# Kernel optimization log

Measured on AMD Instinct MI355X. Metric: run time of the kernel, lower is better.

Reference implementation:

```python
import jax, jax.numpy as jnp
import numpy as np

N_NODES = 50000
N_EDGES = 600000
IN_DIM, HID_DIM, OUT_DIM = 128, 256, 40


def setup_inputs() -> dict:
    key = jax.random.key(0)
    ks = jax.random.split(key, 10)
    x = jax.random.normal(ks[0], (N_NODES, IN_DIM), dtype=jnp.float32)
    edge_index = jax.random.randint(ks[1], (2, N_EDGES), 0, N_NODES, dtype=jnp.int64)
    def lin(k, out_d, in_d):
        s = 1.0 / np.sqrt(in_d)
        return jax.random.uniform(k, (out_d, in_d), jnp.float32, -s, s)
    # SAGEConv: lin_l (on aggregated neighbors, with bias) + lin_r (on self, no bias)
    params = {
        "Wl1": lin(ks[2], HID_DIM, IN_DIM), "bl1": jnp.zeros((HID_DIM,), jnp.float32), "Wr1": lin(ks[3], HID_DIM, IN_DIM),
        "Wl2": lin(ks[4], HID_DIM, HID_DIM), "bl2": jnp.zeros((HID_DIM,), jnp.float32), "Wr2": lin(ks[5], HID_DIM, HID_DIM),
        "Wl3": lin(ks[6], OUT_DIM, HID_DIM), "bl3": jnp.zeros((OUT_DIM,), jnp.float32), "Wr3": lin(ks[7], OUT_DIM, HID_DIM),
    }
    return {"x": x, "edge_index": edge_index, **params}


def _sage_conv(x, src, dst, Wl, bl, Wr):
    # mean-aggregate source features into destination nodes
    n = x.shape[0]
    agg = jax.ops.segment_sum(x[src], dst, num_segments=n)          # [N, d_in]
    cnt = jax.ops.segment_sum(jnp.ones_like(dst, dtype=x.dtype), dst, num_segments=n)
    mean = agg / jnp.maximum(cnt, 1.0)[:, None]
    return mean @ Wl.T + bl + x @ Wr.T


def reference(x, edge_index, Wl1, bl1, Wr1, Wl2, bl2, Wr2, Wl3, bl3, Wr3):
    src, dst = edge_index[0], edge_index[1]
    h = _sage_conv(x, src, dst, Wl1, bl1, Wr1)
    h = jax.nn.relu(h)  # dropout is identity in eval mode
    h = _sage_conv(h, src, dst, Wl2, bl2, Wr2)
    h = jax.nn.relu(h)
    h = _sage_conv(h, src, dst, Wl3, bl3, Wr3)
    return jax.nn.log_softmax(h, axis=1)
```

## Files before the change

### kernel.cpp

```cpp
#include <hip/hip_runtime.h>
#include <hip/hip_bf16.h>

#define IN_DIM 128
#define HID_DIM 256
#define OUT_DIM 40
#define SCAN_CHUNK 2048

typedef __attribute__((ext_vector_type(8))) __bf16 bf16x8;
typedef __attribute__((ext_vector_type(4))) float f32x4;

__device__ inline ushort f2bf(float f) {
    uint u = __builtin_bit_cast(uint, f);
    u = (u + 0x7fff + ((u >> 16) & 1)) >> 16;
    return (ushort)u;
}
__device__ inline float bfl(uint u) { return __builtin_bit_cast(float, u << 16); }
__device__ inline float bfh(uint u) { return __builtin_bit_cast(float, u & 0xffff0000u); }

__global__ __launch_bounds__(256) void cvt_x(const float* __restrict__ in,
                                             ushort* __restrict__ out, int n4) {
    int i = blockIdx.x * 256 + threadIdx.x;
    if (i < n4) {
        float4 v = ((const float4*)in)[i];
        uint2 o;
        o.x = (uint)f2bf(v.x) | ((uint)f2bf(v.y) << 16);
        o.y = (uint)f2bf(v.z) | ((uint)f2bf(v.w) << 16);
        ((uint2*)out)[i] = o;
    }
}

__global__ __launch_bounds__(256) void cvt_w2(const float* __restrict__ wl,
                                              const float* __restrict__ wr,
                                              ushort* __restrict__ ol,
                                              ushort* __restrict__ orr,
                                              int O, int OPAD, int K) {
    int idx = blockIdx.x * 256 + threadIdx.x;
    int tot = OPAD * K;
    if (idx >= tot) return;
    int row = idx / K;
    int col = idx - row * K;
    ushort vl = 0, vr = 0;
    if (row < O) {
        vl = f2bf(wl[row * K + col]);
        vr = f2bf(wr[row * K + col]);
    }
    ol[idx] = vl;
    orr[idx] = vr;
}

__global__ __launch_bounds__(256) void hist_kernel(const int* __restrict__ dst,
                                                   int* __restrict__ cnt, int E) {
    int e = blockIdx.x * 256 + threadIdx.x;
    if (e < E) atomicAdd(&cnt[dst[e]], 1);
}

__global__ __launch_bounds__(256) void scan_pass1(const int* __restrict__ cnt,
                                                  int* __restrict__ bsum, int N) {
    __shared__ int red[256];
    const int base = blockIdx.x * SCAN_CHUNK;
    int s = 0;
    for (int i = threadIdx.x; i < SCAN_CHUNK; i += 256) {
        int idx = base + i;
        if (idx < N) s += cnt[idx];
    }
    red[threadIdx.x] = s;
    __syncthreads();
    for (int o = 128; o > 0; o >>= 1) {
        if (threadIdx.x < o) red[threadIdx.x] += red[threadIdx.x + o];
        __syncthreads();
    }
    if (threadIdx.x == 0) bsum[blockIdx.x] = red[0];
}

__global__ __launch_bounds__(256) void scan_pass2(int* __restrict__ bsum, int B) {
    __shared__ int ls[256];
    const int t = threadIdx.x;
    int v = (t < B) ? bsum[t] : 0;
    ls[t] = v;
    __syncthreads();
    for (int o = 1; o < 256; o <<= 1) {
        int u = (t >= o) ? ls[t - o] : 0;
        __syncthreads();
        ls[t] += u;
        __syncthreads();
    }
    if (t < B) bsum[t] = ls[t] - v;
}

__global__ __launch_bounds__(256) void scan_pass3(const int* __restrict__ cnt,
                                                  const int* __restrict__ bsum,
                                                  int* __restrict__ rowptr,
                                                  int* __restrict__ cursor,
                                                  float* __restrict__ inv, int N, int E) {
    __shared__ int ls[256];
    const int tbase = blockIdx.x * SCAN_CHUNK + threadIdx.x * 8;
    int c[8];
    int s = 0;
#pragma unroll
    for (int j = 0; j < 8; ++j) {
        int idx = tbase + j;
        c[j] = (idx < N) ? cnt[idx] : 0;
        s += c[j];
    }
    ls[threadIdx.x] = s;
    __syncthreads();
    for (int o = 1; o < 256; o <<= 1) {
        int u = (threadIdx.x >= o) ? ls[threadIdx.x - o] : 0;
        __syncthreads();
        ls[threadIdx.x] += u;
        __syncthreads();
    }
    int run = bsum[blockIdx.x] + ls[threadIdx.x] - s;
#pragma unroll
    for (int j = 0; j < 8; ++j) {
        int idx = tbase + j;
        if (idx < N) {
            rowptr[idx] = run;
            cursor[idx] = run;
            inv[idx] = 1.0f / fmaxf((float)c[j], 1.0f);
            run += c[j];
        }
    }
    if (blockIdx.x == 0 && threadIdx.x == 0) rowptr[N] = E;
}

__global__ __launch_bounds__(256) void fill_kernel(const int* __restrict__ src,
                                                   const int* __restrict__ dst,
                                                   int* __restrict__ cursor,
                                                   int* __restrict__ srcs, int E) {
    int e = blockIdx.x * 256 + threadIdx.x;
    if (e < E) {
        int pos = atomicAdd(&cursor[dst[e]], 1);
        srcs[pos] = src[e];
    }
}

template <int D>
__global__ __launch_bounds__(256) void gather_mean_bf(const ushort* __restrict__ feat,
                                                      const int* __restrict__ rowptr,
                                                      const int* __restrict__ srcs,
                                                      const float* __restrict__ inv,
                                                      ushort* __restrict__ out, int N) {
    constexpr int V = D / 64;
    const int wave = threadIdx.x >> 6;
    const int lane = threadIdx.x & 63;
    const int n = blockIdx.x * 4 + wave;
    if (n >= N) return;
    const int beg = rowptr[n];
    const int end = rowptr[n + 1];
    const int col = lane * V;
    float a0 = 0.f, a1 = 0.f, a2 = 0.f, a3 = 0.f;
    int e = beg;
    if constexpr (V == 4) {
        for (; e + 3 < end; e += 4) {
            int s0 = srcs[e], s1 = srcs[e + 1], s2 = srcs[e + 2], s3 = srcs[e + 3];
            uint2 q0 = *(const uint2*)&feat[(long long)s0 * D + col];
            uint2 q1 = *(const uint2*)&feat[(long long)s1 * D + col];
            uint2 q2 = *(const uint2*)&feat[(long long)s2 * D + col];
            uint2 q3 = *(const uint2*)&feat[(long long)s3 * D + col];
            a0 += (bfl(q0.x) + bfl(q1.x)) + (bfl(q2.x) + bfl(q3.x));
            a1 += (bfh(q0.x) + bfh(q1.x)) + (bfh(q2.x) + bfh(q3.x));
            a2 += (bfl(q0.y) + bfl(q1.y)) + (bfl(q2.y) + bfl(q3.y));
            a3 += (bfh(q0.y) + bfh(q1.y)) + (bfh(q2.y) + bfh(q3.y));
        }
        for (; e + 1 < end; e += 2) {
            int s0 = srcs[e], s1 = srcs[e + 1];
            uint2 q0 = *(const uint2*)&feat[(long long)s0 * D + col];
            uint2 q1 = *(const uint2*)&feat[(long long)s1 * D + col];
            a0 += bfl(q0.x) + bfl(q1.x);
            a1 += bfh(q0.x) + bfh(q1.x);
            a2 += bfl(q0.y) + bfl(q1.y);
            a3 += bfh(q0.y) + bfh(q1.y);
        }
        if (e < end) {
            uint2 q0 = *(const uint2*)&feat[(long long)srcs[e] * D + col];
            a0 += bfl(q0.x); a1 += bfh(q0.x); a2 += bfl(q0.y); a3 += bfh(q0.y);
        }
        const float sc = inv[n];
        uint2 o;
        o.x = (uint)f2bf(a0 * sc) | ((uint)f2bf(a1 * sc) << 16);
        o.y = (uint)f2bf(a2 * sc) | ((uint)f2bf(a3 * sc) << 16);
        *(uint2*)&out[(long long)n * D + col] = o;
    } else {
        for (; e + 3 < end; e += 4) {
            int s0 = srcs[e], s1 = srcs[e + 1], s2 = srcs[e + 2], s3 = srcs[e + 3];
            uint q0 = *(const uint*)&feat[(long long)s0 * D + col];
            uint q1 = *(const uint*)&feat[(long long)s1 * D + col];
            uint q2 = *(const uint*)&feat[(long long)s2 * D + col];
            uint q3 = *(const uint*)&feat[(long long)s3 * D + col];
            a0 += (bfl(q0) + bfl(q1)) + (bfl(q2) + bfl(q3));
            a1 += (bfh(q0) + bfh(q1)) + (bfh(q2) + bfh(q3));
        }
        for (; e + 1 < end; e += 2) {
            int s0 = srcs[e], s1 = srcs[e + 1];
            uint q0 = *(const uint*)&feat[(long long)s0 * D + col];
            uint q1 = *(const uint*)&feat[(long long)s1 * D + col];
            a0 += bfl(q0) + bfl(q1);
            a1 += bfh(q0) + bfh(q1);
        }
        if (e < end) {
            uint q0 = *(const uint*)&feat[(long long)srcs[e] * D + col];
            a0 += bfl(q0); a1 += bfh(q0);
        }
        const float sc = inv[n];
        uint o = (uint)f2bf(a0 * sc) | ((uint)f2bf(a1 * sc) << 16);
        *(uint*)&out[(long long)n * D + col] = o;
    }
}

template <int K, bool RELU, bool OUTBF>
__global__ __launch_bounds__(256, 2) void sage_gemm_fused(const ushort* __restrict__ Amean,
                                                          const ushort* __restrict__ Aself,
                                                          const ushort* __restrict__ Wl,
                                                          const float* __restrict__ bias,
                                                          const ushort* __restrict__ Wr,
                                                          void* __restrict__ outv, int N, int O) {
    constexpr int K2 = 2 * K;
    constexpr int KP = K2 + 8;
    constexpr int NK = K2 / 32;
    __shared__ __align__(16) ushort Ws[64 * KP];

    const int tid = threadIdx.x;
    const int wave = tid >> 6;
    const int lane = tid & 63;
    const int ln = lane & 15;
    const int quad = lane >> 4;
    const int bm0 = (blockIdx.x >> 2) * 128;
    const int bn0 = (blockIdx.x & 3) * 64;

    int arow[2];
#pragma unroll
    for (int rt = 0; rt < 2; ++rt) {
        int r = bm0 + wave * 32 + rt * 16 + ln;
        arow[rt] = min(r, N - 1);
    }

#pragma unroll
    for (int i = tid; i < 64 * (K / 8); i += 256) {
        int row = i / (K / 8);
        int c8 = (i % (K / 8)) * 8;
        *(ulonglong2*)&Ws[row * KP + c8] =
            *(const ulonglong2*)&Wl[(long long)(bn0 + row) * K + c8];
        *(ulonglong2*)&Ws[row * KP + K + c8] =
            *(const ulonglong2*)&Wr[(long long)(bn0 + row) * K + c8];
    }

    f32x4 acc[2][4] = {};
    bf16x8 a_cur[2], a_nxt[2];
#pragma unroll
    for (int rt = 0; rt < 2; ++rt)
        a_cur[rt] = *(const bf16x8*)&Amean[(long long)arow[rt] * K + quad * 8];

    __syncthreads();

#pragma unroll
    for (int kk = 0; kk < NK; ++kk) {
        if (kk + 1 < NK) {
            const ushort* __restrict__ An = (kk + 1 < NK / 2) ? Amean : Aself;
            const int ko = ((kk + 1) % (NK / 2)) * 32;
#pragma unroll
            for (int rt = 0; rt < 2; ++rt)
                a_nxt[rt] = *(const bf16x8*)&An[(long long)arow[rt] * K + ko + quad * 8];
        }
#pragma unroll
        for (int ct = 0; ct < 4; ++ct) {
            bf16x8 b = *(const bf16x8*)&Ws[(ct * 16 + ln) * KP + kk * 32 + quad * 8];
#pragma unroll
            for (int rt = 0; rt < 2; ++rt)
                acc[rt][ct] = __builtin_amdgcn_mfma_f32_16x16x32_bf16(a_cur[rt], b, acc[rt][ct], 0, 0, 0);
        }
#pragma unroll
        for (int rt = 0; rt < 2; ++rt) a_cur[rt] = a_nxt[rt];
    }

#pragma unroll
    for (int rt = 0; rt < 2; ++rt) {
        int rbase = bm0 + wave * 32 + rt * 16 + quad * 4;
#pragma unroll
        for (int ct = 0; ct < 4; ++ct) {
            int col = bn0 + ct * 16 + ln;
            if (col >= O) continue;
            float bv = bias[col];
#pragma unroll
            for (int r = 0; r < 4; ++r) {
                int row = rbase + r;
                if (row >= N) continue;
                float v = acc[rt][ct][r] + bv;
                if (RELU) v = fmaxf(v, 0.f);
                if (OUTBF)
                    ((ushort*)outv)[(long long)row * O + col] = f2bf(v);
                else
                    ((float*)outv)[(long long)row * O + col] = v;
            }
        }
    }
}

template <int K>
__global__ __launch_bounds__(256, 2) void sage_gemm_pre(const ushort* __restrict__ A0,
                                                        const ushort* __restrict__ Wl,
                                                        const ushort* __restrict__ Wr,
                                                        ushort* __restrict__ P,
                                                        float* __restrict__ S, int N, int O) {
    constexpr int KP = 2 * K + 8;
    constexpr int NK = K / 32;
    __shared__ __align__(16) ushort Ws[64 * KP];

    const int tid = threadIdx.x;
    const int wave = tid >> 6;
    const int lane = tid & 63;
    const int ln = lane & 15;
    const int quad = lane >> 4;
    const int bm0 = blockIdx.x * 64;

    const int arow = min(bm0 + wave * 16 + ln, N - 1);

    bf16x8 areg[NK];
#pragma unroll
    for (int kk = 0; kk < NK; ++kk)
        areg[kk] = *(const bf16x8*)&A0[(long long)arow * K + kk * 32 + quad * 8];

#pragma unroll
    for (int i = tid; i < 64 * (K / 8); i += 256) {
        int row = i / (K / 8);
        int c8 = (i % (K / 8)) * 8;
        *(ulonglong2*)&Ws[row * KP + c8] =
            *(const ulonglong2*)&Wl[(long long)row * K + c8];
        *(ulonglong2*)&Ws[row * KP + K + c8] =
            *(const ulonglong2*)&Wr[(long long)row * K + c8];
    }
    __syncthreads();

#pragma unroll
    for (int phase = 0; phase < 2; ++phase) {
        f32x4 acc[4] = {};
#pragma unroll
        for (int kk = 0; kk < NK; ++kk) {
#pragma unroll
            for (int ct = 0; ct < 4; ++ct) {
                bf16x8 b = *(const bf16x8*)&Ws[(ct * 16 + ln) * KP + phase * K + kk * 32 + quad * 8];
                acc[ct] = __builtin_amdgcn_mfma_f32_16x16x32_bf16(areg[kk], b, acc[ct], 0, 0, 0);
            }
        }
        int rbase = bm0 + wave * 16 + quad * 4;
#pragma unroll
        for (int ct = 0; ct < 3; ++ct) {
            int col = ct * 16 + ln;
            if (col >= O) continue;
#pragma unroll
            for (int r = 0; r < 4; ++r) {
                int row = rbase + r;
                if (row >= N) continue;
                if (phase == 0)
                    P[(long long)row * O + col] = f2bf(acc[ct][r]);
                else
                    S[(long long)row * O + col] = acc[ct][r];
            }
        }
    }
}

__global__ __launch_bounds__(256) void agg_bias_lsm(const ushort* __restrict__ P,
                                                    const float* __restrict__ S,
                                                    const float* __restrict__ bias,
                                                    const int* __restrict__ rowptr,
                                                    const int* __restrict__ srcs,
                                                    const float* __restrict__ inv,
                                                    float* __restrict__ out, int N) {
    const int wave = threadIdx.x >> 6;
    const int lane = threadIdx.x & 63;
    const int n = blockIdx.x * 4 + wave;
    if (n >= N) return;
    const int beg = rowptr[n];
    const int end = rowptr[n + 1];
    const bool act = lane < OUT_DIM;
    const int cidx = act ? lane : 0;

    float acc = 0.f;
    int e = beg;
    for (; e + 3 < end; e += 4) {
        int s0 = srcs[e], s1 = srcs[e + 1], s2 = srcs[e + 2], s3 = srcs[e + 3];
        float v0 = __builtin_bit_cast(float, (uint)P[(long long)s0 * OUT_DIM + cidx] << 16);
        float v1 = __builtin_bit_cast(float, (uint)P[(long long)s1 * OUT_DIM + cidx] << 16);
        float v2 = __builtin_bit_cast(float, (uint)P[(long long)s2 * OUT_DIM + cidx] << 16);
        float v3 = __builtin_bit_cast(float, (uint)P[(long long)s3 * OUT_DIM + cidx] << 16);
        acc += (v0 + v1) + (v2 + v3);
    }
    for (; e < end; ++e)
        acc += __builtin_bit_cast(float, (uint)P[(long long)srcs[e] * OUT_DIM + cidx] << 16);

    float v = act ? (acc * inv[n] + S[(long long)n * OUT_DIM + lane] + bias[lane]) : -INFINITY;
    float m = v;
#pragma unroll
    for (int o = 32; o > 0; o >>= 1) m = fmaxf(m, __shfl_xor(m, o, 64));
    float ex = act ? expf(v - m) : 0.f;
    float sm = ex;
#pragma unroll
    for (int o = 32; o > 0; o >>= 1) sm += __shfl_xor(sm, o, 64);
    float ls = logf(sm);
    if (act) out[(long long)n * OUT_DIM + lane] = v - m - ls;
}

extern "C" void kernel_launch(void* const* d_in, const int* in_sizes, int n_in,
                              void* d_out, int out_size, void* d_ws, size_t ws_size,
                              hipStream_t stream) {
    const float* x   = (const float*)d_in[0];
    const int*   ei  = (const int*)d_in[1];
    const float* Wl1 = (const float*)d_in[2];
    const float* bl1 = (const float*)d_in[3];
    const float* Wr1 = (const float*)d_in[4];
    const float* Wl2 = (const float*)d_in[5];
    const float* bl2 = (const float*)d_in[6];
    const float* Wr2 = (const float*)d_in[7];
    const float* Wl3 = (const float*)d_in[8];
    const float* bl3 = (const float*)d_in[9];
    const float* Wr3 = (const float*)d_in[10];
    float* out = (float*)d_out;

    const int N = in_sizes[0] / IN_DIM;
    const int E = in_sizes[1] / 2;
    const int* src = ei;
    const int* dst = ei + E;

    char* w = (char*)d_ws;
    size_t off = 0;
    auto alloc = [&](size_t bytes) {
        void* p = w + off;
        off = (off + bytes + 255) & ~(size_t)255;
        return p;
    };
    ushort* xb   = (ushort*)alloc((size_t)N * IN_DIM * 2);
    ushort* M    = (ushort*)alloc((size_t)N * HID_DIM * 2);
    ushort* H1   = (ushort*)alloc((size_t)N * HID_DIM * 2);
    ushort* H2   = (ushort*)alloc((size_t)N * HID_DIM * 2);
    ushort* P3   = (ushort*)alloc((size_t)N * OUT_DIM * 2);
    float*  S3   = (float*)alloc((size_t)N * OUT_DIM * 4);
    float*  inv  = (float*)alloc((size_t)N * 4);
    int*    cnt  = (int*)alloc((size_t)N * 4);
    int*    rowptr = (int*)alloc((size_t)(N + 1) * 4);
    int*    cursor = (int*)alloc((size_t)N * 4);
    int*    srcs = (int*)alloc((size_t)E * 4);
    int*    bsum = (int*)alloc(256 * 4);
    ushort* Wl1b = (ushort*)alloc(256 * 128 * 2);
    ushort* Wr1b = (ushort*)alloc(256 * 128 * 2);
    ushort* Wl2b = (ushort*)alloc(256 * 256 * 2);
    ushort* Wr2b = (ushort*)alloc(256 * 256 * 2);
    ushort* Wl3b = (ushort*)alloc(64 * 256 * 2);
    ushort* Wr3b = (ushort*)alloc(64 * 256 * 2);

    cvt_x<<<(N * IN_DIM / 4 + 255) / 256, 256, 0, stream>>>(x, xb, N * IN_DIM / 4);
    cvt_w2<<<(256 * 128 + 255) / 256, 256, 0, stream>>>(Wl1, Wr1, Wl1b, Wr1b, 256, 256, 128);
    cvt_w2<<<(256 * 256 + 255) / 256, 256, 0, stream>>>(Wl2, Wr2, Wl2b, Wr2b, 256, 256, 256);
    cvt_w2<<<(64 * 256 + 255) / 256, 256, 0, stream>>>(Wl3, Wr3, Wl3b, Wr3b, 40, 64, 256);

    const int SB = (N + SCAN_CHUNK - 1) / SCAN_CHUNK;
    hipMemsetAsync(cnt, 0, (size_t)N * sizeof(int), stream);
    hist_kernel<<<(E + 255) / 256, 256, 0, stream>>>(dst, cnt, E);
    scan_pass1<<<SB, 256, 0, stream>>>(cnt, bsum, N);
    scan_pass2<<<1, 256, 0, stream>>>(bsum, SB);
    scan_pass3<<<SB, 256, 0, stream>>>(cnt, bsum, rowptr, cursor, inv, N, E);
    fill_kernel<<<(E + 255) / 256, 256, 0, stream>>>(src, dst, cursor, srcs, E);

    const int gm = (N + 127) / 128;
    const int gg = (N + 3) / 4;

    gather_mean_bf<IN_DIM><<<gg, 256, 0, stream>>>(xb, rowptr, srcs, inv, M, N);
    sage_gemm_fused<IN_DIM, true, true><<<gm * 4, 256, 0, stream>>>(
        M, xb, Wl1b, bl1, Wr1b, H1, N, HID_DIM);

    gather_mean_bf<HID_DIM><<<gg, 256, 0, stream>>>(H1, rowptr, srcs, inv, M, N);
    sage_gemm_fused<HID_DIM, true, true><<<gm * 4, 256, 0, stream>>>(
        M, H1, Wl2b, bl2, Wr2b, H2, N, HID_DIM);

    sage_gemm_pre<HID_DIM><<<(N + 63) / 64, 256, 0, stream>>>(
        H2, Wl3b, Wr3b, P3, S3, N, OUT_DIM);
    agg_bias_lsm<<<gg, 256, 0, stream>>>(P3, S3, bl3, rowptr, srcs, inv, out, N);
}
```

Measured before the change: 381.0 us.

## Split fused SAGE GEMM into two K phases to halve shared memory

The fused GEMM now stages only one weight matrix (Wl, then Wr) in shared memory per phase instead of both concatenated, which halves LDS use and raises the occupancy target to 3 blocks per CU. It preloads all A fragments for each phase into registers instead of software-pipelining one step ahead. The grid becomes 2D with column tiles on blockIdx.y, which changes the order in which blocks are dispatched. The layer-3 pre-GEMM trims its padded output columns from 64 to 48, cutting LDS and MFMA work. The trade-offs are an extra pair of barriers and weight reload per block, plus higher register pressure from the full A preload.

```diff
diff --git a/kernel.cpp b/kernel.cpp
--- a/kernel.cpp
+++ b/kernel.cpp
@@ -209,15 +209,14 @@
 }
 
 template <int K, bool RELU, bool OUTBF>
-__global__ __launch_bounds__(256, 2) void sage_gemm_fused(const ushort* __restrict__ Amean,
-                                                          const ushort* __restrict__ Aself,
-                                                          const ushort* __restrict__ Wl,
-                                                          const float* __restrict__ bias,
-                                                          const ushort* __restrict__ Wr,
-                                                          void* __restrict__ outv, int N, int O) {
-    constexpr int K2 = 2 * K;
-    constexpr int KP = K2 + 8;
-    constexpr int NK = K2 / 32;
+__global__ __launch_bounds__(256, 3) void sage_gemm_mfma(const ushort* __restrict__ Amean,
+                                                         const ushort* __restrict__ Aself,
+                                                         const ushort* __restrict__ Wl,
+                                                         const float* __restrict__ bias,
+                                                         const ushort* __restrict__ Wr,
+                                                         void* __restrict__ outv, int N, int O) {
+    constexpr int KP = K + 8;
+    constexpr int NK = K / 32;
     __shared__ __align__(16) ushort Ws[64 * KP];
 
     const int tid = threadIdx.x;
@@ -225,8 +224,8 @@
     const int lane = tid & 63;
     const int ln = lane & 15;
     const int quad = lane >> 4;
-    const int bm0 = (blockIdx.x >> 2) * 128;
-    const int bn0 = (blockIdx.x & 3) * 64;
+    const int bm0 = blockIdx.x * 128;
+    const int bn0 = blockIdx.y * 64;
 
     int arow[2];
 #pragma unroll
@@ -235,42 +234,39 @@
         arow[rt] = min(r, N - 1);
     }
 
-#pragma unroll
-    for (int i = tid; i < 64 * (K / 8); i += 256) {
-        int row = i / (K / 8);
-        int c8 = (i % (K / 8)) * 8;
-        *(ulonglong2*)&Ws[row * KP + c8] =
-            *(const ulonglong2*)&Wl[(long long)(bn0 + row) * K + c8];
-        *(ulonglong2*)&Ws[row * KP + K + c8] =
-            *(const ulonglong2*)&Wr[(long long)(bn0 + row) * K + c8];
-    }
-
     f32x4 acc[2][4] = {};
-    bf16x8 a_cur[2], a_nxt[2];
-#pragma unroll
-    for (int rt = 0; rt < 2; ++rt)
-        a_cur[rt] = *(const bf16x8*)&Amean[(long long)arow[rt] * K + quad * 8];
-
-    __syncthreads();
-
-#pragma unroll
-    for (int kk = 0; kk < NK; ++kk) {
-        if (kk + 1 < NK) {
-            const ushort* __restrict__ An = (kk + 1 < NK / 2) ? Amean : Aself;
-            const int ko = ((kk + 1) % (NK / 2)) * 32;
+
+    for (int phase = 0; phase < 2; ++phase) {
+        const ushort* __restrict__ A = phase ? Aself : Amean;
+        const ushort* __restrict__ W = phase ? Wr : Wl;
+
+        __syncthreads();
+#pragma unroll
+        for (int i = tid; i < 64 * (K / 8); i += 256) {
+            int row = i / (K / 8);
+            int c8 = (i % (K / 8)) * 8;
+            *(ulonglong2*)&Ws[row * KP + c8] =
+                *(const ulonglong2*)&W[(long long)(bn0 + row) * K + c8];
+        }
+        __syncthreads();
+
+        bf16x8 areg[NK][2];
+#pragma unroll
+        for (int kk = 0; kk < NK; ++kk)
 #pragma unroll
             for (int rt = 0; rt < 2; ++rt)
-                a_nxt[rt] = *(const bf16x8*)&An[(long long)arow[rt] * K + ko + quad * 8];
-        }
-#pragma unroll
-        for (int ct = 0; ct < 4; ++ct) {
-            bf16x8 b = *(const bf16x8*)&Ws[(ct * 16 + ln) * KP + kk * 32 + quad * 8];
-#pragma unroll
-            for (int rt = 0; rt < 2; ++rt)
-                acc[rt][ct] = __builtin_amdgcn_mfma_f32_16x16x32_bf16(a_cur[rt], b, acc[rt][ct], 0, 0, 0);
-        }
-#pragma unroll
-        for (int rt = 0; rt < 2; ++rt) a_cur[rt] = a_nxt[rt];
+                areg[kk][rt] = *(const bf16x8*)&A[(long long)arow[rt] * K + kk * 32 + quad * 8];
+
+#pragma unroll
+        for (int kk = 0; kk < NK; ++kk) {
+#pragma unroll
+            for (int ct = 0; ct < 4; ++ct) {
+                bf16x8 b = *(const bf16x8*)&Ws[(ct * 16 + ln) * KP + kk * 32 + quad * 8];
+#pragma unroll
+                for (int rt = 0; rt < 2; ++rt)
+                    acc[rt][ct] = __builtin_amdgcn_mfma_f32_16x16x32_bf16(areg[kk][rt], b, acc[rt][ct], 0, 0, 0);
+            }
+        }
     }
 
 #pragma unroll
@@ -297,14 +293,14 @@
 }
 
 template <int K>
-__global__ __launch_bounds__(256, 2) void sage_gemm_pre(const ushort* __restrict__ A0,
+__global__ __launch_bounds__(256, 3) void sage_gemm_pre(const ushort* __restrict__ A0,
                                                         const ushort* __restrict__ Wl,
                                                         const ushort* __restrict__ Wr,
                                                         ushort* __restrict__ P,
                                                         float* __restrict__ S, int N, int O) {
     constexpr int KP = 2 * K + 8;
     constexpr int NK = K / 32;
-    __shared__ __align__(16) ushort Ws[64 * KP];
+    __shared__ __align__(16) ushort Ws[48 * KP];
 
     const int tid = threadIdx.x;
     const int wave = tid >> 6;
@@ -315,13 +311,8 @@
 
     const int arow = min(bm0 + wave * 16 + ln, N - 1);
 
-    bf16x8 areg[NK];
-#pragma unroll
-    for (int kk = 0; kk < NK; ++kk)
-        areg[kk] = *(const bf16x8*)&A0[(long long)arow * K + kk * 32 + quad * 8];
-
-#pragma unroll
-    for (int i = tid; i < 64 * (K / 8); i += 256) {
+#pragma unroll
+    for (int i = tid; i < 48 * (K / 8); i += 256) {
         int row = i / (K / 8);
         int c8 = (i % (K / 8)) * 8;
         *(ulonglong2*)&Ws[row * KP + c8] =
@@ -331,13 +322,18 @@
     }
     __syncthreads();
 
+    bf16x8 areg[NK];
+#pragma unroll
+    for (int kk = 0; kk < NK; ++kk)
+        areg[kk] = *(const bf16x8*)&A0[(long long)arow * K + kk * 32 + quad * 8];
+
 #pragma unroll
     for (int phase = 0; phase < 2; ++phase) {
-        f32x4 acc[4] = {};
+        f32x4 acc[3] = {};
 #pragma unroll
         for (int kk = 0; kk < NK; ++kk) {
 #pragma unroll
-            for (int ct = 0; ct < 4; ++ct) {
+            for (int ct = 0; ct < 3; ++ct) {
                 bf16x8 b = *(const bf16x8*)&Ws[(ct * 16 + ln) * KP + phase * K + kk * 32 + quad * 8];
                 acc[ct] = __builtin_amdgcn_mfma_f32_16x16x32_bf16(areg[kk], b, acc[ct], 0, 0, 0);
             }
@@ -445,13 +441,13 @@
     ushort* Wr1b = (ushort*)alloc(256 * 128 * 2);
     ushort* Wl2b = (ushort*)alloc(256 * 256 * 2);
     ushort* Wr2b = (ushort*)alloc(256 * 256 * 2);
-    ushort* Wl3b = (ushort*)alloc(64 * 256 * 2);
-    ushort* Wr3b = (ushort*)alloc(64 * 256 * 2);
+    ushort* Wl3b = (ushort*)alloc(48 * 256 * 2);
+    ushort* Wr3b = (ushort*)alloc(48 * 256 * 2);
 
     cvt_x<<<(N * IN_DIM / 4 + 255) / 256, 256, 0, stream>>>(x, xb, N * IN_DIM / 4);
     cvt_w2<<<(256 * 128 + 255) / 256, 256, 0, stream>>>(Wl1, Wr1, Wl1b, Wr1b, 256, 256, 128);
     cvt_w2<<<(256 * 256 + 255) / 256, 256, 0, stream>>>(Wl2, Wr2, Wl2b, Wr2b, 256, 256, 256);
-    cvt_w2<<<(64 * 256 + 255) / 256, 256, 0, stream>>>(Wl3, Wr3, Wl3b, Wr3b, 40, 64, 256);
+    cvt_w2<<<(48 * 256 + 255) / 256, 256, 0, stream>>>(Wl3, Wr3, Wl3b, Wr3b, 40, 48, 256);
 
     const int SB = (N + SCAN_CHUNK - 1) / SCAN_CHUNK;
     hipMemsetAsync(cnt, 0, (size_t)N * sizeof(int), stream);
@@ -465,11 +461,11 @@
     const int gg = (N + 3) / 4;
 
     gather_mean_bf<IN_DIM><<<gg, 256, 0, stream>>>(xb, rowptr, srcs, inv, M, N);
-    sage_gemm_fused<IN_DIM, true, true><<<gm * 4, 256, 0, stream>>>(
+    sage_gemm_mfma<IN_DIM, true, true><<<dim3(gm, 4), 256, 0, stream>>>(
         M, xb, Wl1b, bl1, Wr1b, H1, N, HID_DIM);
 
     gather_mean_bf<HID_DIM><<<gg, 256, 0, stream>>>(H1, rowptr, srcs, inv, M, N);
-    sage_gemm_fused<HID_DIM, true, true><<<gm * 4, 256, 0, stream>>>(
+    sage_gemm_mfma<HID_DIM, true, true><<<dim3(gm, 4), 256, 0, stream>>>(
         M, H1, Wl2b, bl2, Wr2b, H2, N, HID_DIM);
 
     sage_gemm_pre<HID_DIM><<<(N + 63) / 64, 256, 0, stream>>>(
```

Result: faster. 368.5 us (-3.3%).
